# Optimization experiments

Measured on AMD Instinct MI355X. Metric: run time of the kernel, lower is better.

The kernel has to match this reference:

```python
import jax, jax.numpy as jnp
import numpy as np
import math

TA = 0.6081734479693927            # tet target angle / pi (109.47 deg)
DELTA_THETA_DEG = 12.0             # tet gaussian width (degrees)


def _plm(l, m, x, s):
    """Associated Legendre P_l^m(x) with Condon-Shortley phase, s = sin(theta)."""
    if l == 2:
        if m == 0: return 0.5 * (3 * x ** 2 - 1)
        if m == 1: return -3.0 * x * s
        return 3.0 * s ** 2
    if l == 4:
        if m == 0: return 0.125 * (35 * x ** 4 - 30 * x ** 2 + 3)
        if m == 1: return -2.5 * (7 * x ** 3 - 3 * x) * s
        if m == 2: return 7.5 * (7 * x ** 2 - 1) * s ** 2
        if m == 3: return -105.0 * x * s ** 3
        return 105.0 * s ** 4
    # l == 6
    if m == 0: return (231 * x ** 6 - 315 * x ** 4 + 105 * x ** 2 - 5) / 16.0
    if m == 1: return -(21.0 / 8.0) * (33 * x ** 5 - 30 * x ** 3 + 5 * x) * s
    if m == 2: return (105.0 / 8.0) * (33 * x ** 4 - 18 * x ** 2 + 1) * s ** 2
    if m == 3: return -(315.0 / 2.0) * (11 * x ** 3 - 3 * x) * s ** 3
    if m == 4: return (945.0 / 2.0) * (11 * x ** 2 - 1) * s ** 4
    if m == 5: return -10395.0 * x * s ** 5
    return 10395.0 * s ** 6


def _ql(l, theta, phi, mask, nb):
    """Steinhardt bond-orientational order parameter q_l, shape (M,)."""
    x = jnp.cos(theta)
    s = jnp.sin(theta)  # theta in [0, pi] so s >= 0
    acc = 0.0
    for m in range(l + 1):
        nlm = math.sqrt((2 * l + 1) / (4 * math.pi)
                        * math.factorial(l - m) / math.factorial(l + m))
        P = nlm * _plm(l, m, x, s)                      # (M, K)
        re = jnp.sum(P * jnp.cos(m * phi) * mask, axis=1) / nb
        im = jnp.sum(P * jnp.sin(m * phi) * mask, axis=1) / nb
        w = 1.0 if m == 0 else 2.0                      # |Y_{l,-m}| = |Y_{l,m}|
        acc = acc + w * (re ** 2 + im ** 2)
    return jnp.sqrt(4 * math.pi / (2 * l + 1) * acc)


def _forward(positions, atom_indices, neighbor_indices, valid_mask):
    mask = valid_mask.astype(positions.dtype)           # (M, K)
    maskb = valid_mask > 0
    safe_idx = jnp.where(maskb, neighbor_indices, 0)
    neigh_pos = positions[safe_idx]                     # (M, K, 3) gather
    center = positions[atom_indices]                    # (M, 3)

    vec = neigh_pos - center[:, None, :]
    dist = jnp.linalg.norm(vec, axis=-1)                # (M, K)
    unit = vec / (dist[..., None] + 1e-10)
    cos_t = jnp.clip(unit[..., 2], -1.0 + 1e-7, 1.0 - 1e-7)
    theta = jnp.arccos(cos_t) * mask
    phi = jnp.arctan2(unit[..., 1], unit[..., 0]) * mask
    unit = unit * mask[..., None]

    cn = jnp.sum(mask, axis=1)                          # coordination number
    nb = jnp.maximum(cn, 1.0)

    # tetrahedral OP: gaussian of pairwise neighbor-neighbor angles
    K = mask.shape[1]
    cos_ang = jnp.clip(jnp.einsum('mkd,mld->mkl', unit, unit),
                       -1.0 + 1e-7, 1.0 - 1e-7)
    ang = jnp.arccos(cos_ang)                           # (M, K, K)
    pair_mask = (mask[:, :, None] * mask[:, None, :]
                 * (1.0 - jnp.eye(K, dtype=mask.dtype)))
    theta_t = TA * math.pi
    sigma = DELTA_THETA_DEG * math.pi / 180.0
    gauss = jnp.exp(-0.5 * ((ang - theta_t) / sigma) ** 2) * pair_mask
    n_pairs = jnp.maximum(cn * (cn - 1.0), 1.0)
    tet = jnp.sum(gauss, axis=(1, 2)) / n_pairs

    q2 = _ql(2, theta, phi, mask, nb)
    q4 = _ql(4, theta, phi, mask, nb)
    q6 = _ql(6, theta, phi, mask, nb)
    return cn, tet, q2, q4, q6


def setup_inputs() -> dict:
    key = jax.random.key(0)
    k0, k1, k2, k3 = jax.random.split(key, 4)
    N, M, K = 80000, 80000, 20
    positions = jax.random.normal(k0, (N, 3), dtype=jnp.float32)
    atom_indices = jax.random.randint(k1, (M,), 0, N, dtype=jnp.int32)
    neighbor_indices = jax.random.randint(k2, (M, K), 0, N, dtype=jnp.int32)
    valid_mask = jax.random.randint(k3, (M, K), 0, 2, dtype=jnp.int32)
    return {"positions": positions, "atom_indices": atom_indices,
            "neighbor_indices": neighbor_indices, "valid_mask": valid_mask}


def reference(positions, atom_indices, neighbor_indices, valid_mask):
    return _forward(positions, atom_indices, neighbor_indices, valid_mask)
```

## Files before the change

kernel.cpp:

```cpp
#include <hip/hip_runtime.h>
#include <math.h>

#define KNBR 20
#define BLK  256
#define GRP  16
#define APB  (BLK / GRP)
#define MAXP 190
#define PERSIST 2048
#define GLUT 1024

#define THETA_T  1.9106332362490186f
#define INV_SIG  4.7746482927568605f
#define PI_F     3.14159265358979323846f

__global__ __launch_bounds__(BLK, 8)
void op_kernel(const float* __restrict__ pos,
               const int*   __restrict__ aidx,
               const int*   __restrict__ nidx,
               const int*   __restrict__ vmsk,
               float*       __restrict__ out,
               int M, int NT)
{
    __shared__ float4 su[APB * KNBR];
    __shared__ unsigned short lut[MAXP];
    __shared__ float glut[GLUT + 1];

    const int tid = threadIdx.x;
    if (tid < MAXP) {
        const int j = (int)((1.0f + sqrtf(fmaf(8.f, (float)tid, 1.0f))) * 0.5f);
        lut[tid] = (unsigned short)((tid - ((j * (j - 1)) >> 1)) | (j << 8));
    }
    for (int k = tid; k <= GLUT; k += BLK) {
        const float d  = fmaf((float)k, 2.0f / GLUT, -1.0f);
        const float dc = fminf(fmaxf(d, -0.9999999f), 0.9999999f);
        const float ad = fabsf(dc);
        const float pq = fmaf(fmaf(fmaf(-0.0187293f, ad, 0.0742610f), ad,
                              -0.2121144f), ad, 1.5707288f) * sqrtf(1.f - ad);
        const float ang = (dc >= 0.f) ? pq : PI_F - pq;
        const float tt = (ang - THETA_T) * INV_SIG;
        glut[k] = __expf(-0.5f * tt * tt);
    }
    __syncthreads();

    const int r   = tid & (GRP - 1);
    const int g   = tid / GRP;
    const int sub = (tid & 63) >> 4;
    float4* row = &su[g * KNBR];

    int t = blockIdx.x;
    if (t >= NT) return;

    int i = t * APB + g;
    int is = min(i, M - 1);
    int a  = aidx[is];
    size_t ri = (size_t)is * KNBR;
    int n0 = nidx[ri + r];
    int v0 = (i < M) ? vmsk[ri + r] : 0;
    int n1 = 0, v1 = 0;
    if (r < 4) { n1 = nidx[ri + 16 + r]; v1 = (i < M) ? vmsk[ri + 16 + r] : 0; }

    while (true) {
        const int tn = t + gridDim.x;
        int aN = 0, n0N = 0, v0N = 0, n1N = 0, v1N = 0, iN = 0;
        if (tn < NT) {
            iN = tn * APB + g;
            const int isN = min(iN, M - 1);
            aN = aidx[isN];
            const size_t rN = (size_t)isN * KNBR;
            n0N = nidx[rN + r];
            v0N = (iN < M) ? vmsk[rN + r] : 0;
            if (r < 4) { n1N = nidx[rN + 16 + r]; v1N = (iN < M) ? vmsk[rN + 16 + r] : 0; }
        }

        const int use1 = (r < 4) & (v1 != 0);
        const int s0i = (v0 != 0) ? n0 : 0;
        const int s1i = use1 ? n1 : 0;
        const float cx = pos[3*a], cy = pos[3*a+1], cz = pos[3*a+2];
        const float p0x = pos[3*s0i], p0y = pos[3*s0i+1], p0z = pos[3*s0i+2];
        const float p1x = pos[3*s1i], p1y = pos[3*s1i+1], p1z = pos[3*s1i+2];

        const unsigned long long bal0 = __ballot(v0 != 0);
        const unsigned long long bal1 = __ballot(use1 != 0);
        const unsigned int b16 = (unsigned int)(bal0 >> (sub * 16)) & 0xFFFFu;
        const unsigned int c4  = (unsigned int)(bal1 >> (sub * 16)) & 0xFu;
        const unsigned int mask20 = b16 | (c4 << 16);
        const int total = __popc(mask20);

        if (v0 != 0) {
            const float vx = p0x - cx, vy = p0y - cy, vz = p0z - cz;
            const float d2 = fmaf(vx, vx, fmaf(vy, vy, vz * vz));
            const int   zed = d2 < 1e-24f;
            const float inv = __builtin_amdgcn_rcpf(sqrtf(d2) + 1e-10f);
            const int slot = __popc(mask20 & ((1u << r) - 1u));
            row[slot] = make_float4(zed ? 1.f : vx * inv,
                                    zed ? 0.f : vy * inv,
                                    zed ? 0.f : vz * inv,
                                    zed ? 0.f : 1.f);
        }
        if (use1) {
            const float vx = p1x - cx, vy = p1y - cy, vz = p1z - cz;
            const float d2 = fmaf(vx, vx, fmaf(vy, vy, vz * vz));
            const int   zed = d2 < 1e-24f;
            const float inv = __builtin_amdgcn_rcpf(sqrtf(d2) + 1e-10f);
            const int slot = __popc(mask20 & ((1u << (16 + r)) - 1u));
            row[slot] = make_float4(zed ? 1.f : vx * inv,
                                    zed ? 0.f : vy * inv,
                                    zed ? 0.f : vz * inv,
                                    zed ? 0.f : 1.f);
        }

        const int npairs = (total * (total - 1)) >> 1;
        float m1 = 0.f, m2 = 0.f, m3 = 0.f, gsum = 0.f;
        for (int p = r; p < npairs; p += GRP) {
            const unsigned short w = lut[p];
            const float4 A = row[w & 0xFF];
            const float4 B = row[w >> 8];
            const float dsh = fmaf(A.x, B.x, fmaf(A.y, B.y, A.z * B.z));
            const float dtt = dsh * A.w * B.w;

            const float e  = dsh * dsh;
            const float e2 = e * e;
            m1 += e;
            m2 += e2;
            m3 = fmaf(e2, e, m3);

            float fx = fmaf(dtt, (float)(GLUT / 2), (float)(GLUT / 2));
            fx = fminf(fmaxf(fx, 0.f), (float)GLUT - 0.0001f);
            const int   k  = (int)fx;
            const float fr = fx - (float)k;
            const float g0 = glut[k];
            const float g1 = glut[k + 1];
            gsum += fmaf(fr, g1 - g0, g0);
        }

#define RED(v) { v += __shfl_xor(v,1); v += __shfl_xor(v,2); \
                 v += __shfl_xor(v,4); v += __shfl_xor(v,8); }
        RED(m1) RED(m2) RED(m3) RED(gsum)
#undef RED

        const float fnp = (float)npairs;
        const float s2 = fmaf(1.5f, m1, -0.5f * fnp);
        const float s4 = fmaf(4.375f, m2, fmaf(-3.75f, m1, 0.375f * fnp));
        const float s6 = fmaf(14.4375f, m3,
                         fmaf(-19.6875f, m2, fmaf(6.5625f, m1, -0.3125f * fnp)));

        const float cn = (float)total;
        const float invnb = 1.f / fmaxf(cn, 1.f);
        const float tet = 2.f * gsum / fmaxf(cn * (cn - 1.f), 1.f);
        const float q2v = invnb * sqrtf(fmaxf(fmaf(2.f, s2, cn), 0.f));
        const float q4v = invnb * sqrtf(fmaxf(fmaf(2.f, s4, cn), 0.f));
        const float q6v = invnb * sqrtf(fmaxf(fmaf(2.f, s6, cn), 0.f));

        float val = cn;
        val = (r == 1) ? tet : val;
        val = (r == 2) ? q2v : val;
        val = (r == 3) ? q4v : val;
        val = (r == 4) ? q6v : val;
        if (r < 5 && i < M)
            out[r * M + i] = val;

        if (tn >= NT) break;
        t = tn; i = iN; a = aN;
        n0 = n0N; v0 = v0N; n1 = n1N; v1 = v1N;
    }
}

extern "C" void kernel_launch(void* const* d_in, const int* in_sizes, int n_in,
                              void* d_out, int out_size, void* d_ws, size_t ws_size,
                              hipStream_t stream) {
    const float* pos  = (const float*)d_in[0];
    const int*   aidx = (const int*)d_in[1];
    const int*   nidx = (const int*)d_in[2];
    const int*   vmsk = (const int*)d_in[3];
    float* out = (float*)d_out;
    const int M = in_sizes[1];
    const int NT = (M + APB - 1) / APB;
    const int grid = NT < PERSIST ? NT : PERSIST;
    op_kernel<<<grid, BLK, 0, stream>>>(pos, aidx, nidx, vmsk, out, M, NT);
}
```

Before: 19.62 us.

## Use 8-lane groups per atom, nearest-neighbor gauss LUT, exact-tile specialization

Halves the lanes per atom from 16 to 8, so each block processes 32 atoms and each lane handles up to three neighbor slots, with three ballots used to build the compaction mask. The Gaussian lookup switches from linear interpolation to nearest-entry rounding, cutting one LDS load and some ALU per pair. A template flag removes bounds checks when M divides evenly into tiles, 32-bit indexing replaces size_t, and the final divisions become rcp intrinsics. The pair loop now runs up to 190/8 iterations per lane instead of 190/16, trading more serial work per lane for more atoms in flight, and nearest lookup adds some approximation error to tet.

Result: faster. 16.72 us (-14.8%).

```diff
diff --git a/kernel.cpp b/kernel.cpp
--- a/kernel.cpp
+++ b/kernel.cpp
@@ -3,7 +3,7 @@
 
 #define KNBR 20
 #define BLK  256
-#define GRP  16
+#define GRP  8
 #define APB  (BLK / GRP)
 #define MAXP 190
 #define PERSIST 2048
@@ -13,6 +13,18 @@
 #define INV_SIG  4.7746482927568605f
 #define PI_F     3.14159265358979323846f
 
+__device__ __forceinline__ float gauss_at(int k) {
+    const float d  = fmaf((float)k, 2.0f / GLUT, -1.0f);
+    const float dc = fminf(fmaxf(d, -0.9999999f), 0.9999999f);
+    const float ad = fabsf(dc);
+    const float pq = fmaf(fmaf(fmaf(-0.0187293f, ad, 0.0742610f), ad,
+                          -0.2121144f), ad, 1.5707288f) * sqrtf(1.f - ad);
+    const float ang = (dc >= 0.f) ? pq : PI_F - pq;
+    const float tt = (ang - THETA_T) * INV_SIG;
+    return __expf(-0.5f * tt * tt);
+}
+
+template<bool EXACT>
 __global__ __launch_bounds__(BLK, 8)
 void op_kernel(const float* __restrict__ pos,
                const int*   __restrict__ aidx,
@@ -30,60 +42,60 @@
         const int j = (int)((1.0f + sqrtf(fmaf(8.f, (float)tid, 1.0f))) * 0.5f);
         lut[tid] = (unsigned short)((tid - ((j * (j - 1)) >> 1)) | (j << 8));
     }
-    for (int k = tid; k <= GLUT; k += BLK) {
-        const float d  = fmaf((float)k, 2.0f / GLUT, -1.0f);
-        const float dc = fminf(fmaxf(d, -0.9999999f), 0.9999999f);
-        const float ad = fabsf(dc);
-        const float pq = fmaf(fmaf(fmaf(-0.0187293f, ad, 0.0742610f), ad,
-                              -0.2121144f), ad, 1.5707288f) * sqrtf(1.f - ad);
-        const float ang = (dc >= 0.f) ? pq : PI_F - pq;
-        const float tt = (ang - THETA_T) * INV_SIG;
-        glut[k] = __expf(-0.5f * tt * tt);
-    }
+    for (int k = tid; k <= GLUT; k += BLK)
+        glut[k] = gauss_at(k);
     __syncthreads();
 
     const int r   = tid & (GRP - 1);
     const int g   = tid / GRP;
-    const int sub = (tid & 63) >> 4;
+    const int sub = (tid & 63) >> 3;
     float4* row = &su[g * KNBR];
 
     int t = blockIdx.x;
     if (t >= NT) return;
 
     int i = t * APB + g;
-    int is = min(i, M - 1);
+    int is = EXACT ? i : min(i, M - 1);
     int a  = aidx[is];
-    size_t ri = (size_t)is * KNBR;
+    int ri = is * KNBR;
     int n0 = nidx[ri + r];
-    int v0 = (i < M) ? vmsk[ri + r] : 0;
-    int n1 = 0, v1 = 0;
-    if (r < 4) { n1 = nidx[ri + 16 + r]; v1 = (i < M) ? vmsk[ri + 16 + r] : 0; }
+    int v0 = (EXACT || i < M) ? vmsk[ri + r] : 0;
+    int n1 = nidx[ri + 8 + r];
+    int v1 = (EXACT || i < M) ? vmsk[ri + 8 + r] : 0;
+    int n2 = 0, v2 = 0;
+    if (r < 4) { n2 = nidx[ri + 16 + r]; v2 = (EXACT || i < M) ? vmsk[ri + 16 + r] : 0; }
 
     while (true) {
         const int tn = t + gridDim.x;
-        int aN = 0, n0N = 0, v0N = 0, n1N = 0, v1N = 0, iN = 0;
+        int aN = 0, n0N = 0, v0N = 0, n1N = 0, v1N = 0, n2N = 0, v2N = 0, iN = 0;
         if (tn < NT) {
             iN = tn * APB + g;
-            const int isN = min(iN, M - 1);
+            const int isN = EXACT ? iN : min(iN, M - 1);
             aN = aidx[isN];
-            const size_t rN = (size_t)isN * KNBR;
+            const int rN = isN * KNBR;
             n0N = nidx[rN + r];
-            v0N = (iN < M) ? vmsk[rN + r] : 0;
-            if (r < 4) { n1N = nidx[rN + 16 + r]; v1N = (iN < M) ? vmsk[rN + 16 + r] : 0; }
-        }
-
-        const int use1 = (r < 4) & (v1 != 0);
+            v0N = (EXACT || iN < M) ? vmsk[rN + r] : 0;
+            n1N = nidx[rN + 8 + r];
+            v1N = (EXACT || iN < M) ? vmsk[rN + 8 + r] : 0;
+            if (r < 4) { n2N = nidx[rN + 16 + r]; v2N = (EXACT || iN < M) ? vmsk[rN + 16 + r] : 0; }
+        }
+
+        const int use2 = (r < 4) & (v2 != 0);
         const int s0i = (v0 != 0) ? n0 : 0;
-        const int s1i = use1 ? n1 : 0;
-        const float cx = pos[3*a], cy = pos[3*a+1], cz = pos[3*a+2];
+        const int s1i = (v1 != 0) ? n1 : 0;
+        const int s2i = use2 ? n2 : 0;
+        const float cx  = pos[3*a],   cy  = pos[3*a+1],   cz  = pos[3*a+2];
         const float p0x = pos[3*s0i], p0y = pos[3*s0i+1], p0z = pos[3*s0i+2];
         const float p1x = pos[3*s1i], p1y = pos[3*s1i+1], p1z = pos[3*s1i+2];
+        const float p2x = pos[3*s2i], p2y = pos[3*s2i+1], p2z = pos[3*s2i+2];
 
         const unsigned long long bal0 = __ballot(v0 != 0);
-        const unsigned long long bal1 = __ballot(use1 != 0);
-        const unsigned int b16 = (unsigned int)(bal0 >> (sub * 16)) & 0xFFFFu;
-        const unsigned int c4  = (unsigned int)(bal1 >> (sub * 16)) & 0xFu;
-        const unsigned int mask20 = b16 | (c4 << 16);
+        const unsigned long long bal1 = __ballot(v1 != 0);
+        const unsigned long long bal2 = __ballot(use2 != 0);
+        const unsigned int b0 = (unsigned int)(bal0 >> (sub * 8)) & 0xFFu;
+        const unsigned int b1 = (unsigned int)(bal1 >> (sub * 8)) & 0xFFu;
+        const unsigned int b2 = (unsigned int)(bal2 >> (sub * 8)) & 0xFu;
+        const unsigned int mask20 = b0 | (b1 << 8) | (b2 << 16);
         const int total = __popc(mask20);
 
         if (v0 != 0) {
@@ -97,8 +109,19 @@
                                     zed ? 0.f : vz * inv,
                                     zed ? 0.f : 1.f);
         }
-        if (use1) {
+        if (v1 != 0) {
             const float vx = p1x - cx, vy = p1y - cy, vz = p1z - cz;
+            const float d2 = fmaf(vx, vx, fmaf(vy, vy, vz * vz));
+            const int   zed = d2 < 1e-24f;
+            const float inv = __builtin_amdgcn_rcpf(sqrtf(d2) + 1e-10f);
+            const int slot = __popc(mask20 & ((1u << (8 + r)) - 1u));
+            row[slot] = make_float4(zed ? 1.f : vx * inv,
+                                    zed ? 0.f : vy * inv,
+                                    zed ? 0.f : vz * inv,
+                                    zed ? 0.f : 1.f);
+        }
+        if (use2) {
+            const float vx = p2x - cx, vy = p2y - cy, vz = p2z - cz;
             const float d2 = fmaf(vx, vx, fmaf(vy, vy, vz * vz));
             const int   zed = d2 < 1e-24f;
             const float inv = __builtin_amdgcn_rcpf(sqrtf(d2) + 1e-10f);
@@ -124,17 +147,12 @@
             m2 += e2;
             m3 = fmaf(e2, e, m3);
 
-            float fx = fmaf(dtt, (float)(GLUT / 2), (float)(GLUT / 2));
-            fx = fminf(fmaxf(fx, 0.f), (float)GLUT - 0.0001f);
-            const int   k  = (int)fx;
-            const float fr = fx - (float)k;
-            const float g0 = glut[k];
-            const float g1 = glut[k + 1];
-            gsum += fmaf(fr, g1 - g0, g0);
-        }
-
-#define RED(v) { v += __shfl_xor(v,1); v += __shfl_xor(v,2); \
-                 v += __shfl_xor(v,4); v += __shfl_xor(v,8); }
+            float fx = fmaf(dtt, (float)(GLUT / 2), (float)(GLUT / 2) + 0.5f);
+            fx = fminf(fmaxf(fx, 0.f), (float)GLUT + 0.49f);
+            gsum += glut[(int)fx];
+        }
+
+#define RED(v) { v += __shfl_xor(v,1); v += __shfl_xor(v,2); v += __shfl_xor(v,4); }
         RED(m1) RED(m2) RED(m3) RED(gsum)
 #undef RED
 
@@ -145,8 +163,8 @@
                          fmaf(-19.6875f, m2, fmaf(6.5625f, m1, -0.3125f * fnp)));
 
         const float cn = (float)total;
-        const float invnb = 1.f / fmaxf(cn, 1.f);
-        const float tet = 2.f * gsum / fmaxf(cn * (cn - 1.f), 1.f);
+        const float invnb = __builtin_amdgcn_rcpf(fmaxf(cn, 1.f));
+        const float tet = gsum * __builtin_amdgcn_rcpf(fmaxf(fnp, 0.5f));
         const float q2v = invnb * sqrtf(fmaxf(fmaf(2.f, s2, cn), 0.f));
         const float q4v = invnb * sqrtf(fmaxf(fmaf(2.f, s4, cn), 0.f));
         const float q6v = invnb * sqrtf(fmaxf(fmaf(2.f, s6, cn), 0.f));
@@ -156,12 +174,12 @@
         val = (r == 2) ? q2v : val;
         val = (r == 3) ? q4v : val;
         val = (r == 4) ? q6v : val;
-        if (r < 5 && i < M)
+        if (r < 5 && (EXACT || i < M))
             out[r * M + i] = val;
 
         if (tn >= NT) break;
         t = tn; i = iN; a = aN;
-        n0 = n0N; v0 = v0N; n1 = n1N; v1 = v1N;
+        n0 = n0N; v0 = v0N; n1 = n1N; v1 = v1N; n2 = n2N; v2 = v2N;
     }
 }
 
@@ -176,5 +194,8 @@
     const int M = in_sizes[1];
     const int NT = (M + APB - 1) / APB;
     const int grid = NT < PERSIST ? NT : PERSIST;
-    op_kernel<<<grid, BLK, 0, stream>>>(pos, aidx, nidx, vmsk, out, M, NT);
+    if (M % APB == 0)
+        op_kernel<true><<<grid, BLK, 0, stream>>>(pos, aidx, nidx, vmsk, out, M, NT);
+    else
+        op_kernel<false><<<grid, BLK, 0, stream>>>(pos, aidx, nidx, vmsk, out, M, NT);
 }
```
